# Optimization experiments

Hardware: AMD Instinct MI355X
Metric: run time of the kernel (lower is better)

## Reference

```python
import jax, jax.numpy as jnp
import numpy as np
import math

B, C, HW = 4, 256, 32          # batch, seq_len (=channels), spatial side
D_MODEL = HW * HW              # 1024
OUT_C = 32 * 32                # 1024
D_STATE = 16
EXPAND = 2
D_INNER = EXPAND * D_MODEL     # 2048
DT_RANK = math.ceil(D_MODEL / 16)  # 64
D_CONV = 4


def setup_inputs() -> dict:
    key = jax.random.key(0)
    ks = jax.random.split(key, 12)
    s = 0.02
    x1 = jax.random.normal(ks[0], (B, C, HW, HW), dtype=jnp.float32)
    in_proj_w = jax.random.normal(ks[1], (2 * D_INNER, D_MODEL), dtype=jnp.float32) * s
    conv_w = jax.random.normal(ks[2], (D_INNER, 1, D_CONV), dtype=jnp.float32) * s
    conv_b = jnp.zeros((D_INNER,), dtype=jnp.float32)
    x_proj_w = jax.random.normal(ks[3], (DT_RANK + 2 * D_STATE, D_INNER), dtype=jnp.float32) * s
    dt_proj_w = jax.random.normal(ks[4], (D_INNER, DT_RANK), dtype=jnp.float32) * s
    dt_proj_b = jnp.zeros((D_INNER,), dtype=jnp.float32)
    A_log = jnp.log(jnp.broadcast_to(jnp.arange(1, D_STATE + 1, dtype=jnp.float32), (D_INNER, D_STATE)))
    D = jnp.ones((D_INNER,), dtype=jnp.float32)
    out_proj_w = jax.random.normal(ks[5], (OUT_C, D_INNER), dtype=jnp.float32) * s
    ln_w = jnp.ones((OUT_C,), dtype=jnp.float32)
    ln_b = jnp.zeros((OUT_C,), dtype=jnp.float32)
    return {"x1": x1, "in_proj_w": in_proj_w, "conv_w": conv_w, "conv_b": conv_b,
            "x_proj_w": x_proj_w, "dt_proj_w": dt_proj_w, "dt_proj_b": dt_proj_b,
            "A_log": A_log, "D": D, "out_proj_w": out_proj_w, "ln_w": ln_w, "ln_b": ln_b}


def _mamba_forward(x, in_proj_w, conv_w, conv_b, x_proj_w, dt_proj_w, dt_proj_b, A_log, D, out_proj_w):
    # x: (B, L, d_model)
    xz = jnp.einsum('bld,ed->ble', x, in_proj_w)            # (B,L,2*d_inner)
    xs, res = jnp.split(xz, 2, axis=-1)                     # each (B,L,d_inner)
    # depthwise causal conv1d, padding=d_conv-1 then truncate to L (== left pad)
    xs_c = jnp.transpose(xs, (0, 2, 1))                     # (B,d_inner,L)
    xs_c = jax.lax.conv_general_dilated(
        xs_c, conv_w, window_strides=(1,), padding=[(D_CONV - 1, 0)],
        dimension_numbers=('NCH', 'OIH', 'NCH'), feature_group_count=D_INNER)
    xs_c = xs_c + conv_b[None, :, None]
    xs = jax.nn.silu(jnp.transpose(xs_c, (0, 2, 1)))        # (B,L,d_inner)
    # input-dependent SSM parameters
    x_dbl = jnp.einsum('bld,ed->ble', xs, x_proj_w)         # (B,L,dt_rank+2N)
    dt, Bm, Cm = jnp.split(x_dbl, [DT_RANK, DT_RANK + D_STATE], axis=-1)
    delta = jax.nn.softplus(jnp.einsum('blr,dr->bld', dt, dt_proj_w) + dt_proj_b)  # (B,L,d_inner)
    A = -jnp.exp(A_log)                                     # (d_inner, N)
    deltaA = jnp.exp(delta[..., None] * A)                  # (B,L,d_inner,N)
    deltaB_u = delta[..., None] * Bm[:, :, None, :] * xs[..., None]  # (B,L,d_inner,N)

    def step(h, inp):
        dA, dBu, Ct = inp                                   # (B,d,N),(B,d,N),(B,N)
        h = dA * h + dBu
        y = jnp.einsum('bdn,bn->bd', h, Ct)
        return h, y

    h0 = jnp.zeros((deltaA.shape[0], D_INNER, D_STATE), dtype=deltaA.dtype)
    _, ys = jax.lax.scan(step, h0, (jnp.transpose(deltaA, (1, 0, 2, 3)),
                                    jnp.transpose(deltaB_u, (1, 0, 2, 3)),
                                    jnp.transpose(Cm, (1, 0, 2))))
    y = jnp.transpose(ys, (1, 0, 2))                        # (B,L,d_inner)
    y = y + D * xs
    y = y * jax.nn.silu(res)
    return jnp.einsum('bld,od->blo', y, out_proj_w)         # (B,L,out_c)


def reference(x1, in_proj_w, conv_w, conv_b, x_proj_w, dt_proj_w, dt_proj_b,
              A_log, D, out_proj_w, ln_w, ln_b):
    b, c, h, w = x1.shape
    x = x1.reshape(b, c, h * w)                             # (B, L=c, d_model)
    y = _mamba_forward(x, in_proj_w, conv_w, conv_b, x_proj_w, dt_proj_w,
                       dt_proj_b, A_log, D, out_proj_w)
    mu = jnp.mean(y, axis=-1, keepdims=True)
    var = jnp.var(y, axis=-1, keepdims=True)
    y = (y - mu) * jax.lax.rsqrt(var + 1e-5) * ln_w + ln_b
    return y.reshape(b, c, 32, 32)
```

## Files before the change

### kernel.cpp

```cpp
#include <hip/hip_runtime.h>
#include <hip/hip_bf16.h>
#include <math.h>

#define BATCH 4
#define SEQL 256
#define DMODEL 1024
#define DINNER 2048
#define DSTATE 16
#define DTRANK 64
#define OUTC 1024
#define NROWS (BATCH * SEQL)
#define NCHUNK 4
#define CH 64

typedef __attribute__((ext_vector_type(8))) short bf16x8;
typedef __attribute__((ext_vector_type(4))) float f32x4;

__global__ __launch_bounds__(256) void gemm_mfma(const __hip_bfloat16* __restrict__ A,
                                                 const __hip_bfloat16* __restrict__ B,
                                                 float* __restrict__ C,
                                                 int M, int N, int K,
                                                 int lda, int ldb) {
    __shared__ __hip_bfloat16 As[4][128 * 32];
    __shared__ __hip_bfloat16 Bs[4][128 * 32];
    const int t  = threadIdx.x;
    const int w  = t >> 6;
    const int ln = t & 63;
    const int wm = w >> 1, wn = w & 1;
    const int q  = ln >> 4, lr = ln & 15;
    const int m0 = blockIdx.y * 128;
    const int n0 = blockIdx.x * 128;
    const int Kpart = K / gridDim.z;
    const int kbase = blockIdx.z * Kpart;

    f32x4 acc[4][4] = {};

    const __hip_bfloat16* Ag = A + (size_t)m0 * lda + kbase;
    const __hip_bfloat16* Bg = B + (size_t)n0 * ldb + kbase;

    auto stage = [&](int k0, int buf) {
        #pragma unroll
        for (int i = 0; i < 2; ++i) {
            const int c = (i * 4 + w) * 64 + ln;
            const int r = c >> 2, col = (c & 3) * 8;
            __builtin_amdgcn_global_load_lds(
                (const __attribute__((address_space(1))) void*)(Ag + (size_t)r * lda + k0 + col),
                (__attribute__((address_space(3))) void*)(As[buf] + (i * 4 + w) * 64 * 8),
                16, 0, 0);
            __builtin_amdgcn_global_load_lds(
                (const __attribute__((address_space(1))) void*)(Bg + (size_t)r * ldb + k0 + col),
                (__attribute__((address_space(3))) void*)(Bs[buf] + (i * 4 + w) * 64 * 8),
                16, 0, 0);
        }
    };

    const int nk = Kpart / 32;
    for (int s = 0; s < 3 && s < nk; ++s) stage(s * 32, s);

    for (int kk = 0; kk < nk; ++kk) {
        const int last = (kk + 2 < nk - 1) ? (kk + 2) : (nk - 1);
        const int nf = last - kk;
        if (nf >= 2)      asm volatile("s_waitcnt vmcnt(8)" ::: "memory");
        else if (nf == 1) asm volatile("s_waitcnt vmcnt(4)" ::: "memory");
        else              asm volatile("s_waitcnt vmcnt(0)" ::: "memory");
        __builtin_amdgcn_s_barrier();
        if (kk + 3 < nk) stage((kk + 3) * 32, (kk + 3) & 3);

        const int buf = kk & 3;
        bf16x8 af[4], bfr[4];
        #pragma unroll
        for (int i = 0; i < 4; ++i)
            af[i] = *(const bf16x8*)(As[buf] + (wm * 64 + i * 16 + lr) * 32 + q * 8);
        #pragma unroll
        for (int j = 0; j < 4; ++j)
            bfr[j] = *(const bf16x8*)(Bs[buf] + (wn * 64 + j * 16 + lr) * 32 + q * 8);
        #pragma unroll
        for (int i = 0; i < 4; ++i)
            #pragma unroll
            for (int j = 0; j < 4; ++j)
                acc[i][j] = __builtin_amdgcn_mfma_f32_16x16x32_bf16(af[i], bfr[j], acc[i][j], 0, 0, 0);
    }
    float* Cz = C + (size_t)blockIdx.z * M * N;
    #pragma unroll
    for (int i = 0; i < 4; ++i) {
        const int mrow = m0 + wm * 64 + i * 16 + q * 4;
        #pragma unroll
        for (int j = 0; j < 4; ++j) {
            const int ncol = n0 + wn * 64 + j * 16 + lr;
            #pragma unroll
            for (int r = 0; r < 4; ++r)
                Cz[(size_t)(mrow + r) * N + ncol] = acc[i][j][r];
        }
    }
}

__global__ __launch_bounds__(256) void gemm_dtsp(const __hip_bfloat16* __restrict__ A,
                                                 const __hip_bfloat16* __restrict__ B,
                                                 const float* __restrict__ bd,
                                                 float* __restrict__ delta) {
    __shared__ __hip_bfloat16 As[2][128 * 32];
    __shared__ __hip_bfloat16 Bs[2][128 * 32];
    const int t  = threadIdx.x;
    const int w  = t >> 6;
    const int ln = t & 63;
    const int wm = w >> 1, wn = w & 1;
    const int q  = ln >> 4, lr = ln & 15;
    const int m0 = blockIdx.y * 128;
    const int n0 = blockIdx.x * 128;
    const int lda = 128, ldb = 64, N = 2048;

    f32x4 acc[4][4] = {};
    const __hip_bfloat16* Ag = A + (size_t)m0 * lda;
    const __hip_bfloat16* Bg = B + (size_t)n0 * ldb;

    auto stage = [&](int k0, int buf) {
        #pragma unroll
        for (int i = 0; i < 2; ++i) {
            const int c = (i * 4 + w) * 64 + ln;
            const int r = c >> 2, col = (c & 3) * 8;
            __builtin_amdgcn_global_load_lds(
                (const __attribute__((address_space(1))) void*)(Ag + (size_t)r * lda + k0 + col),
                (__attribute__((address_space(3))) void*)(As[buf] + (i * 4 + w) * 64 * 8),
                16, 0, 0);
            __builtin_amdgcn_global_load_lds(
                (const __attribute__((address_space(1))) void*)(Bg + (size_t)r * ldb + k0 + col),
                (__attribute__((address_space(3))) void*)(Bs[buf] + (i * 4 + w) * 64 * 8),
                16, 0, 0);
        }
    };

    stage(0, 0);
    stage(32, 1);
    #pragma unroll
    for (int kk = 0; kk < 2; ++kk) {
        if (kk == 0) asm volatile("s_waitcnt vmcnt(4)" ::: "memory");
        else         asm volatile("s_waitcnt vmcnt(0)" ::: "memory");
        __builtin_amdgcn_s_barrier();
        bf16x8 af[4], bfr[4];
        #pragma unroll
        for (int i = 0; i < 4; ++i)
            af[i] = *(const bf16x8*)(As[kk] + (wm * 64 + i * 16 + lr) * 32 + q * 8);
        #pragma unroll
        for (int j = 0; j < 4; ++j)
            bfr[j] = *(const bf16x8*)(Bs[kk] + (wn * 64 + j * 16 + lr) * 32 + q * 8);
        #pragma unroll
        for (int i = 0; i < 4; ++i)
            #pragma unroll
            for (int j = 0; j < 4; ++j)
                acc[i][j] = __builtin_amdgcn_mfma_f32_16x16x32_bf16(af[i], bfr[j], acc[i][j], 0, 0, 0);
    }
    #pragma unroll
    for (int i = 0; i < 4; ++i) {
        const int mrow = m0 + wm * 64 + i * 16 + q * 4;
        #pragma unroll
        for (int j = 0; j < 4; ++j) {
            const int ncol = n0 + wn * 64 + j * 16 + lr;
            const float bias = bd[ncol];
            #pragma unroll
            for (int r = 0; r < 4; ++r) {
                float v = acc[i][j][r] + bias;
                float sp = (v > 20.f) ? v : log1pf(__expf(v));
                delta[(size_t)(mrow + r) * N + ncol] = sp;
            }
        }
    }
}

__global__ void xdbl_reduce_kernel(const float* __restrict__ part,
                                   float* __restrict__ xdbl,
                                   __hip_bfloat16* __restrict__ xdblb) {
    const int i = blockIdx.x * 256 + threadIdx.x;
    float s = 0.f;
    #pragma unroll
    for (int z = 0; z < 8; ++z) s += part[(size_t)z * (1024 * 128) + i];
    xdbl[i] = s;
    xdblb[i] = __float2bfloat16(s);
}

#define R0 (1024 * 1024)
#define R1 (R0 + 4096 * 1024)
#define R2 (R1 + 2048 * 1024)
#define R3 (R2 + 128 * 2048)
#define R4 (R3 + 2048 * 64)
__global__ void cast_all_kernel(const float* __restrict__ x1,
                                const float* __restrict__ w_in,
                                const float* __restrict__ w_out,
                                const float* __restrict__ w_xp,
                                const float* __restrict__ w_dt,
                                __hip_bfloat16* __restrict__ xa,
                                __hip_bfloat16* __restrict__ wb1,
                                __hip_bfloat16* __restrict__ wob,
                                __hip_bfloat16* __restrict__ wpb,
                                __hip_bfloat16* __restrict__ wdb) {
    int i = blockIdx.x * 256 + threadIdx.x;
    if (i < R0) {
        xa[i] = __float2bfloat16(x1[i]);
    } else if (i < R1) {
        int j = i - R0; wb1[j] = __float2bfloat16(w_in[j]);
    } else if (i < R2) {
        int j = i - R1; wob[j] = __float2bfloat16(w_out[j]);
    } else if (i < R3) {
        int j = i - R2; int e = j >> 11;
        wpb[j] = __float2bfloat16(e < 96 ? w_xp[j] : 0.f);
    } else if (i < R4) {
        int j = i - R3; wdb[j] = __float2bfloat16(w_dt[j]);
    }
}

__global__ void conv_silu_kernel(const float* __restrict__ xz,
                                 const float* __restrict__ conv_w,
                                 const float* __restrict__ conv_b,
                                 float* __restrict__ xs,
                                 __hip_bfloat16* __restrict__ xsb) {
    int idx = blockIdx.x * blockDim.x + threadIdx.x;
    int d = idx & (DINNER - 1);
    int l = (idx >> 11) & (SEQL - 1);
    int b = idx >> 19;
    const float w0 = conv_w[d * 4 + 0];
    const float w1 = conv_w[d * 4 + 1];
    const float w2 = conv_w[d * 4 + 2];
    const float w3 = conv_w[d * 4 + 3];
    float acc = conv_b[d];
    const size_t base = (size_t)(b * SEQL) * (2 * DINNER) + d;
    if (l >= 3) acc += w0 * xz[base + (size_t)(l - 3) * (2 * DINNER)];
    if (l >= 2) acc += w1 * xz[base + (size_t)(l - 2) * (2 * DINNER)];
    if (l >= 1) acc += w2 * xz[base + (size_t)(l - 1) * (2 * DINNER)];
    acc += w3 * xz[base + (size_t)l * (2 * DINNER)];
    float v = acc / (1.f + __expf(-acc));
    xs[idx] = v;
    xsb[idx] = __float2bfloat16(v);
}

__device__ __forceinline__ float row_reduce16(float x) {
    x += __int_as_float(__builtin_amdgcn_update_dpp(0, __float_as_int(x), 0x128, 0xF, 0xF, true));
    x += __int_as_float(__builtin_amdgcn_update_dpp(0, __float_as_int(x), 0x124, 0xF, 0xF, true));
    x += __int_as_float(__builtin_amdgcn_update_dpp(0, __float_as_int(x), 0x122, 0xF, 0xF, true));
    x += __int_as_float(__builtin_amdgcn_update_dpp(0, __float_as_int(x), 0x121, 0xF, 0xF, true));
    return x;
}

__global__ __launch_bounds__(256) void scan_carry_kernel(const float* __restrict__ delta,
                                                         const float* __restrict__ xs,
                                                         const float* __restrict__ xdbl,
                                                         const float* __restrict__ A_log,
                                                         float* __restrict__ carryL,
                                                         float* __restrict__ carryP) {
    __shared__ float sDU[CH][16][2];
    __shared__ float sB[CH][16];
    const int b = blockIdx.y, c = blockIdx.z, dg = blockIdx.x;
    const int t = threadIdx.x;
    const int dl = t >> 4, n = t & 15;
    const int d = dg * 16 + dl;
    const float a = -__expf(A_log[d * DSTATE + n]);
    const int srow = t >> 4, scol = t & 15;
    const int sd = dg * 16 + scol;
    const int rowbase = b * SEQL + c * CH;
    #pragma unroll
    for (int i = 0; i < 4; ++i) {
        const int row = rowbase + i * 16 + srow;
        const float dv = delta[(size_t)row * DINNER + sd];
        const float xv = xs[(size_t)row * DINNER + sd];
        sDU[i * 16 + srow][scol][0] = dv;
        sDU[i * 16 + srow][scol][1] = dv * xv;
        sB[i * 16 + srow][scol] = xdbl[row * 128 + 64 + scol];
    }
    __syncthreads();
    float h = 0.f, P = 1.f;
    #pragma unroll 16
    for (int l = 0; l < CH; ++l) {
        const float e = __expf(sDU[l][dl][0] * a);
        h = e * h + sDU[l][dl][1] * sB[l][n];
        P *= e;
    }
    const size_t ci = (((size_t)(b * NCHUNK + c)) * DINNER + d) * DSTATE + n;
    carryL[ci] = h;
    carryP[ci] = P;
}

__global__ __launch_bounds__(256) void scan_apply_kernel(const float* __restrict__ delta,
                                                         const float* __restrict__ xs,
                                                         const float* __restrict__ xdbl,
                                                         const float* __restrict__ xz,
                                                         const float* __restrict__ A_log,
                                                         const float* __restrict__ Dp,
                                                         const float* __restrict__ carryL,
                                                         const float* __restrict__ carryP,
                                                         __hip_bfloat16* __restrict__ ybb) {
    __shared__ float sDU[CH][16][2];
    __shared__ float sBC[CH][16][2];
    __shared__ float sGW[CH][16][2];
    const int b = blockIdx.y, c = blockIdx.z, dg = blockIdx.x;
    const int t = threadIdx.x;
    const int dl = t >> 4, n = t & 15;
    const int d = dg * 16 + dl;
    const float a = -__expf(A_log[d * DSTATE + n]);
    const int srow = t >> 4, scol = t & 15;
    const int sd = dg * 16 + scol;
    const float Dstage = Dp[sd];
    const int rowbase = b * SEQL + c * CH;
    #pragma unroll
    for (int i = 0; i < 4; ++i) {
        const int row = rowbase + i * 16 + srow;
        const float dv = delta[(size_t)row * DINNER + sd];
        const float xv = xs[(size_t)row * DINNER + sd];
        const float r  = xz[(size_t)row * (2 * DINNER) + DINNER + sd];
        const float g = r / (1.f + __expf(-r));
        const int lr_ = i * 16 + srow;
        sDU[lr_][scol][0] = dv;
        sDU[lr_][scol][1] = dv * xv;
        sGW[lr_][scol][0] = g;
        sGW[lr_][scol][1] = Dstage * xv * g;
        sBC[lr_][scol][0] = xdbl[row * 128 + 64 + scol];
        sBC[lr_][scol][1] = xdbl[row * 128 + 80 + scol];
    }
    __syncthreads();
    float h = 0.f;
    for (int j = 0; j < c; ++j) {
        const size_t ci = (((size_t)(b * NCHUNK + j)) * DINNER + d) * DSTATE + n;
        h = carryP[ci] * h + carryL[ci];
    }
    #pragma unroll 16
    for (int l = 0; l < CH; ++l) {
        const float e = __expf(sDU[l][dl][0] * a);
        h = e * h + sDU[l][dl][1] * sBC[l][n][0];
        float p = row_reduce16(h * sBC[l][n][1]);
        if (n == 0) {
            const float y = p * sGW[l][dl][0] + sGW[l][dl][1];
            ybb[(size_t)(rowbase + l) * DINNER + d] = __float2bfloat16(y);
        }
    }
}

__global__ __launch_bounds__(256) void ln_kernel(const float* __restrict__ opart,
                                                 const float* __restrict__ lw,
                                                 const float* __restrict__ lb,
                                                 float* __restrict__ out) {
    __shared__ float red[8];
    const int row = blockIdx.x;
    const int t = threadIdx.x;
    float v[4];
    float s = 0.f, s2 = 0.f;
    #pragma unroll
    for (int i = 0; i < 4; ++i) {
        const int c = t + 256 * i;
        float acc = 0.f;
        #pragma unroll
        for (int z = 0; z < 4; ++z)
            acc += opart[(size_t)z * (1024 * 1024) + (size_t)row * OUTC + c];
        v[i] = acc;
        s += acc;
        s2 += acc * acc;
    }
    #pragma unroll
    for (int o = 32; o; o >>= 1) {
        s += __shfl_down(s, o);
        s2 += __shfl_down(s2, o);
    }
    const int wid = t >> 6;
    if ((t & 63) == 0) { red[wid] = s; red[4 + wid] = s2; }
    __syncthreads();
    if (t == 0) {
        float ts = red[0] + red[1] + red[2] + red[3];
        float ts2 = red[4] + red[5] + red[6] + red[7];
        float mu = ts * (1.f / OUTC);
        float var = ts2 * (1.f / OUTC) - mu * mu;
        red[0] = mu;
        red[1] = rsqrtf(var + 1e-5f);
    }
    __syncthreads();
    const float mu = red[0], rs = red[1];
    #pragma unroll
    for (int i = 0; i < 4; ++i) {
        const int c = t + 256 * i;
        out[(size_t)row * OUTC + c] = (v[i] - mu) * rs * lw[c] + lb[c];
    }
}

extern "C" void kernel_launch(void* const* d_in, const int* in_sizes, int n_in,
                              void* d_out, int out_size, void* d_ws, size_t ws_size,
                              hipStream_t stream) {
    const float* x1        = (const float*)d_in[0];
    const float* in_proj_w = (const float*)d_in[1];
    const float* conv_w    = (const float*)d_in[2];
    const float* conv_b    = (const float*)d_in[3];
    const float* x_proj_w  = (const float*)d_in[4];
    const float* dt_proj_w = (const float*)d_in[5];
    const float* dt_proj_b = (const float*)d_in[6];
    const float* A_log     = (const float*)d_in[7];
    const float* Dp        = (const float*)d_in[8];
    const float* out_proj_w= (const float*)d_in[9];
    const float* ln_w      = (const float*)d_in[10];
    const float* ln_b      = (const float*)d_in[11];
    float* out = (float*)d_out;

    char* p = (char*)d_ws;
    __hip_bfloat16* xa    = (__hip_bfloat16*)p; p += (size_t)1024 * 1024 * 2;
    __hip_bfloat16* wb1   = (__hip_bfloat16*)p; p += (size_t)4096 * 1024 * 2;
    __hip_bfloat16* wpb   = (__hip_bfloat16*)p; p += (size_t)128 * 2048 * 2;
    __hip_bfloat16* wob   = (__hip_bfloat16*)p; p += (size_t)1024 * 2048 * 2;
    __hip_bfloat16* wdb   = (__hip_bfloat16*)p; p += (size_t)2048 * 64 * 2;
    __hip_bfloat16* xsb   = (__hip_bfloat16*)p; p += (size_t)1024 * 2048 * 2;
    __hip_bfloat16* ybb   = (__hip_bfloat16*)p; p += (size_t)1024 * 2048 * 2;
    __hip_bfloat16* xdblb = (__hip_bfloat16*)p; p += (size_t)1024 * 128 * 2;
    float* xz    = (float*)p; p += (size_t)1024 * 4096 * 4;
    float* xs    = (float*)p; p += (size_t)1024 * 2048 * 4;
    float* xdbl  = (float*)p; p += (size_t)1024 * 128 * 4;
    float* xpart = (float*)p; p += (size_t)8 * 1024 * 128 * 4;
    float* delta = (float*)p; p += (size_t)1024 * 2048 * 4;
    float* carryL = (float*)p; p += (size_t)BATCH * NCHUNK * DINNER * DSTATE * 4;
    float* carryP = (float*)p; p += (size_t)BATCH * NCHUNK * DINNER * DSTATE * 4;
    float* opart = xz;

    cast_all_kernel<<<(R4 + 255) / 256, 256, 0, stream>>>(x1, in_proj_w, out_proj_w,
                                                          x_proj_w, dt_proj_w,
                                                          xa, wb1, wob, wpb, wdb);
    gemm_mfma<<<dim3(32, 8, 1), 256, 0, stream>>>(xa, wb1, xz,
                                                  NROWS, 2 * DINNER, DMODEL, DMODEL, DMODEL);
    conv_silu_kernel<<<(NROWS * DINNER) / 256, 256, 0, stream>>>(xz, conv_w, conv_b, xs, xsb);
    gemm_mfma<<<dim3(1, 8, 8), 256, 0, stream>>>(xsb, wpb, xpart,
                                                 NROWS, 128, DINNER, DINNER, DINNER);
    xdbl_reduce_kernel<<<(1024 * 128) / 256, 256, 0, stream>>>(xpart, xdbl, xdblb);
    gemm_dtsp<<<dim3(16, 8), 256, 0, stream>>>(xdblb, wdb, dt_proj_b, delta);
    scan_carry_kernel<<<dim3(DINNER / 16, BATCH, NCHUNK), 256, 0, stream>>>(
        delta, xs, xdbl, A_log, carryL, carryP);
    scan_apply_kernel<<<dim3(DINNER / 16, BATCH, NCHUNK), 256, 0, stream>>>(
        delta, xs, xdbl, xz, A_log, Dp, carryL, carryP, ybb);
    gemm_mfma<<<dim3(8, 8, 4), 256, 0, stream>>>(ybb, wob, opart,
                                                 NROWS, OUTC, DINNER, DINNER, DINNER);
    ln_kernel<<<NROWS, 256, 0, stream>>>(opart, ln_w, ln_b, out);
}
```

Baseline: 220.0 us.

## Fuse conv+SiLU into x_proj GEMM and scan; merge chunked scan into one kernel

Removes the standalone conv_silu kernel. The depthwise causal conv and SiLU are now recomputed inside a new x_proj GEMM kernel, with split-K raised to 16, and again inside the scan. The two-pass chunked scan (carry kernel plus apply kernel) becomes one kernel that walks all four chunks sequentially per block. This drops several launches and the xs/xsb/carry buffers, at the cost of redundant conv work and fewer scan blocks (512 instead of 2048), so each block's sequential scan runs four times longer.

```diff
diff --git a/kernel.cpp b/kernel.cpp
--- a/kernel.cpp
+++ b/kernel.cpp
@@ -7,11 +7,11 @@
 #define DMODEL 1024
 #define DINNER 2048
 #define DSTATE 16
-#define DTRANK 64
 #define OUTC 1024
 #define NROWS (BATCH * SEQL)
 #define NCHUNK 4
 #define CH 64
+#define XPZ 16
 
 typedef __attribute__((ext_vector_type(8))) short bf16x8;
 typedef __attribute__((ext_vector_type(4))) float f32x4;
@@ -94,6 +94,106 @@
     }
 }
 
+__global__ __launch_bounds__(256) void xproj_conv(const float* __restrict__ xz,
+                                                  const float* __restrict__ conv_w,
+                                                  const float* __restrict__ conv_b,
+                                                  const __hip_bfloat16* __restrict__ Wp,
+                                                  float* __restrict__ xpart) {
+    __shared__ __hip_bfloat16 As[4 * 4096];
+    __shared__ __hip_bfloat16 Bs[4 * 4096];
+    const int t  = threadIdx.x;
+    const int w  = t >> 6;
+    const int ln = t & 63;
+    const int wm = w >> 1, wn = w & 1;
+    const int q  = ln >> 4, lr = ln & 15;
+    const int z  = blockIdx.x;
+    const int m0 = blockIdx.y * 128;
+    const int kbase = z * 128;
+
+    const __hip_bfloat16* Bg = Wp + kbase;
+    #pragma unroll
+    for (int stg = 0; stg < 4; ++stg) {
+        #pragma unroll
+        for (int i = 0; i < 2; ++i) {
+            const int c = (i * 4 + w) * 64 + ln;
+            const int r = c >> 2, col = (c & 3) * 8;
+            __builtin_amdgcn_global_load_lds(
+                (const __attribute__((address_space(1))) void*)(Bg + (size_t)r * 2048 + stg * 32 + col),
+                (__attribute__((address_space(3))) void*)(Bs + stg * 4096 + (i * 4 + w) * 512),
+                16, 0, 0);
+        }
+    }
+
+    {
+        const int r  = t >> 1;
+        const int dh = (t & 1) * 16;
+        const int gr = m0 + r;
+        const int bb = gr >> 8, l = gr & 255;
+        const float* xrow = xz + (size_t)bb * 256 * 4096;
+        #pragma unroll
+        for (int stg = 0; stg < 4; ++stg) {
+            const int d0 = kbase + stg * 32 + dh;
+            #pragma unroll
+            for (int j = 0; j < 4; ++j) {
+                const int d = d0 + j * 4;
+                float4 t0 = {}, t1 = {}, t2 = {}, t3;
+                if (l >= 3) t0 = *(const float4*)(xrow + (size_t)(l - 3) * 4096 + d);
+                if (l >= 2) t1 = *(const float4*)(xrow + (size_t)(l - 2) * 4096 + d);
+                if (l >= 1) t2 = *(const float4*)(xrow + (size_t)(l - 1) * 4096 + d);
+                t3 = *(const float4*)(xrow + (size_t)l * 4096 + d);
+                const float* p0 = (const float*)&t0;
+                const float* p1 = (const float*)&t1;
+                const float* p2 = (const float*)&t2;
+                const float* p3 = (const float*)&t3;
+                #pragma unroll
+                for (int u = 0; u < 4; ++u) {
+                    const int du = d + u;
+                    const float4 wv = *(const float4*)(conv_w + (size_t)du * 4);
+                    float acc = conv_b[du];
+                    if (l >= 3) acc += wv.x * p0[u];
+                    if (l >= 2) acc += wv.y * p1[u];
+                    if (l >= 1) acc += wv.z * p2[u];
+                    acc += wv.w * p3[u];
+                    const float v = acc / (1.f + __expf(-acc));
+                    As[stg * 4096 + r * 32 + dh + j * 4 + u] = __float2bfloat16(v);
+                }
+            }
+        }
+    }
+    __syncthreads();
+
+    f32x4 acc[4][4] = {};
+    #pragma unroll
+    for (int kk = 0; kk < 4; ++kk) {
+        const __hip_bfloat16* Ab = As + kk * 4096;
+        const __hip_bfloat16* Bb = Bs + kk * 4096;
+        bf16x8 af[4], bfr[4];
+        #pragma unroll
+        for (int i = 0; i < 4; ++i)
+            af[i] = *(const bf16x8*)(Ab + (wm * 64 + i * 16 + lr) * 32 + q * 8);
+        #pragma unroll
+        for (int j = 0; j < 4; ++j)
+            bfr[j] = *(const bf16x8*)(Bb + (wn * 64 + j * 16 + lr) * 32 + q * 8);
+        #pragma unroll
+        for (int i = 0; i < 4; ++i)
+            #pragma unroll
+            for (int j = 0; j < 4; ++j)
+                acc[i][j] = __builtin_amdgcn_mfma_f32_16x16x32_bf16(af[i], bfr[j], acc[i][j], 0, 0, 0);
+    }
+    float* Cz = xpart + (size_t)z * (1024 * 128);
+    #pragma unroll
+    for (int i = 0; i < 4; ++i) {
+        const int mrow = m0 + wm * 64 + i * 16 + q * 4;
+        #pragma unroll
+        for (int j = 0; j < 4; ++j) {
+            const int ncol = wn * 64 + j * 16 + lr;
+            #pragma unroll
+            for (int r = 0; r < 4; ++r)
+                Cz[(size_t)(mrow + r) * 128 + ncol] = acc[i][j][r];
+        }
+    }
+}
+
 __global__ __launch_bounds__(256) void gemm_dtsp(const __hip_bfloat16* __restrict__ A,
                                                  const __hip_bfloat16* __restrict__ B,
                                                  const float* __restrict__ bd,
@@ -172,7 +272,7 @@
     const int i = blockIdx.x * 256 + threadIdx.x;
     float s = 0.f;
     #pragma unroll
-    for (int z = 0; z < 8; ++z) s += part[(size_t)z * (1024 * 128) + i];
+    for (int z = 0; z < XPZ; ++z) s += part[(size_t)z * (1024 * 128) + i];
     xdbl[i] = s;
     xdblb[i] = __float2bfloat16(s);
 }
@@ -207,30 +307,6 @@
     }
 }
 
-__global__ void conv_silu_kernel(const float* __restrict__ xz,
-                                 const float* __restrict__ conv_w,
-                                 const float* __restrict__ conv_b,
-                                 float* __restrict__ xs,
-                                 __hip_bfloat16* __restrict__ xsb) {
-    int idx = blockIdx.x * blockDim.x + threadIdx.x;
-    int d = idx & (DINNER - 1);
-    int l = (idx >> 11) & (SEQL - 1);
-    int b = idx >> 19;
-    const float w0 = conv_w[d * 4 + 0];
-    const float w1 = conv_w[d * 4 + 1];
-    const float w2 = conv_w[d * 4 + 2];
-    const float w3 = conv_w[d * 4 + 3];
-    float acc = conv_b[d];
-    const size_t base = (size_t)(b * SEQL) * (2 * DINNER) + d;
-    if (l >= 3) acc += w0 * xz[base + (size_t)(l - 3) * (2 * DINNER)];
-    if (l >= 2) acc += w1 * xz[base + (size_t)(l - 2) * (2 * DINNER)];
-    if (l >= 1) acc += w2 * xz[base + (size_t)(l - 1) * (2 * DINNER)];
-    acc += w3 * xz[base + (size_t)l * (2 * DINNER)];
-    float v = acc / (1.f + __expf(-acc));
-    xs[idx] = v;
-    xsb[idx] = __float2bfloat16(v);
-}
-
 __device__ __forceinline__ float row_reduce16(float x) {
     x += __int_as_float(__builtin_amdgcn_update_dpp(0, __float_as_int(x), 0x128, 0xF, 0xF, true));
     x += __int_as_float(__builtin_amdgcn_update_dpp(0, __float_as_int(x), 0x124, 0xF, 0xF, true));
@@ -239,57 +315,18 @@
     return x;
 }
 
-__global__ __launch_bounds__(256) void scan_carry_kernel(const float* __restrict__ delta,
-                                                         const float* __restrict__ xs,
-                                                         const float* __restrict__ xdbl,
-                                                         const float* __restrict__ A_log,
-                                                         float* __restrict__ carryL,
-                                                         float* __restrict__ carryP) {
-    __shared__ float sDU[CH][16][2];
-    __shared__ float sB[CH][16];
-    const int b = blockIdx.y, c = blockIdx.z, dg = blockIdx.x;
-    const int t = threadIdx.x;
-    const int dl = t >> 4, n = t & 15;
-    const int d = dg * 16 + dl;
-    const float a = -__expf(A_log[d * DSTATE + n]);
-    const int srow = t >> 4, scol = t & 15;
-    const int sd = dg * 16 + scol;
-    const int rowbase = b * SEQL + c * CH;
-    #pragma unroll
-    for (int i = 0; i < 4; ++i) {
-        const int row = rowbase + i * 16 + srow;
-        const float dv = delta[(size_t)row * DINNER + sd];
-        const float xv = xs[(size_t)row * DINNER + sd];
-        sDU[i * 16 + srow][scol][0] = dv;
-        sDU[i * 16 + srow][scol][1] = dv * xv;
-        sB[i * 16 + srow][scol] = xdbl[row * 128 + 64 + scol];
-    }
-    __syncthreads();
-    float h = 0.f, P = 1.f;
-    #pragma unroll 16
-    for (int l = 0; l < CH; ++l) {
-        const float e = __expf(sDU[l][dl][0] * a);
-        h = e * h + sDU[l][dl][1] * sB[l][n];
-        P *= e;
-    }
-    const size_t ci = (((size_t)(b * NCHUNK + c)) * DINNER + d) * DSTATE + n;
-    carryL[ci] = h;
-    carryP[ci] = P;
-}
-
-__global__ __launch_bounds__(256) void scan_apply_kernel(const float* __restrict__ delta,
-                                                         const float* __restrict__ xs,
-                                                         const float* __restrict__ xdbl,
-                                                         const float* __restrict__ xz,
-                                                         const float* __restrict__ A_log,
-                                                         const float* __restrict__ Dp,
-                                                         const float* __restrict__ carryL,
-                                                         const float* __restrict__ carryP,
-                                                         __hip_bfloat16* __restrict__ ybb) {
+__global__ __launch_bounds__(256) void scan_fused(const float* __restrict__ delta,
+                                                  const float* __restrict__ xz,
+                                                  const float* __restrict__ conv_w,
+                                                  const float* __restrict__ conv_b,
+                                                  const float* __restrict__ xdbl,
+                                                  const float* __restrict__ A_log,
+                                                  const float* __restrict__ Dp,
+                                                  __hip_bfloat16* __restrict__ ybb) {
     __shared__ float sDU[CH][16][2];
     __shared__ float sBC[CH][16][2];
     __shared__ float sGW[CH][16][2];
-    const int b = blockIdx.y, c = blockIdx.z, dg = blockIdx.x;
+    const int b = blockIdx.y, dg = blockIdx.x;
     const int t = threadIdx.x;
     const int dl = t >> 4, n = t & 15;
     const int d = dg * 16 + dl;
@@ -297,36 +334,48 @@
     const int srow = t >> 4, scol = t & 15;
     const int sd = dg * 16 + scol;
     const float Dstage = Dp[sd];
-    const int rowbase = b * SEQL + c * CH;
-    #pragma unroll
-    for (int i = 0; i < 4; ++i) {
-        const int row = rowbase + i * 16 + srow;
-        const float dv = delta[(size_t)row * DINNER + sd];
-        const float xv = xs[(size_t)row * DINNER + sd];
-        const float r  = xz[(size_t)row * (2 * DINNER) + DINNER + sd];
-        const float g = r / (1.f + __expf(-r));
-        const int lr_ = i * 16 + srow;
-        sDU[lr_][scol][0] = dv;
-        sDU[lr_][scol][1] = dv * xv;
-        sGW[lr_][scol][0] = g;
-        sGW[lr_][scol][1] = Dstage * xv * g;
-        sBC[lr_][scol][0] = xdbl[row * 128 + 64 + scol];
-        sBC[lr_][scol][1] = xdbl[row * 128 + 80 + scol];
-    }
-    __syncthreads();
+    const float cb = conv_b[sd];
+    const float w0 = conv_w[sd * 4 + 0];
+    const float w1 = conv_w[sd * 4 + 1];
+    const float w2 = conv_w[sd * 4 + 2];
+    const float w3 = conv_w[sd * 4 + 3];
+    const float* xbase = xz + (size_t)(b * SEQL) * 4096 + sd;
+
     float h = 0.f;
-    for (int j = 0; j < c; ++j) {
-        const size_t ci = (((size_t)(b * NCHUNK + j)) * DINNER + d) * DSTATE + n;
-        h = carryP[ci] * h + carryL[ci];
-    }
-    #pragma unroll 16
-    for (int l = 0; l < CH; ++l) {
-        const float e = __expf(sDU[l][dl][0] * a);
-        h = e * h + sDU[l][dl][1] * sBC[l][n][0];
-        float p = row_reduce16(h * sBC[l][n][1]);
-        if (n == 0) {
-            const float y = p * sGW[l][dl][0] + sGW[l][dl][1];
-            ybb[(size_t)(rowbase + l) * DINNER + d] = __float2bfloat16(y);
+    for (int c = 0; c < NCHUNK; ++c) {
+        const int rowbase = b * SEQL + c * CH;
+        __syncthreads();
+        #pragma unroll
+        for (int i = 0; i < 4; ++i) {
+            const int row = rowbase + i * 16 + srow;
+            const int l = row & (SEQL - 1);
+            const float dv = delta[(size_t)row * DINNER + sd];
+            float acc = cb;
+            if (l >= 3) acc += w0 * xbase[(size_t)(l - 3) * 4096];
+            if (l >= 2) acc += w1 * xbase[(size_t)(l - 2) * 4096];
+            if (l >= 1) acc += w2 * xbase[(size_t)(l - 1) * 4096];
+            acc += w3 * xbase[(size_t)l * 4096];
+            const float xv = acc / (1.f + __expf(-acc));
+            const float r  = xz[(size_t)row * 4096 + DINNER + sd];
+            const float g = r / (1.f + __expf(-r));
+            const int lr_ = i * 16 + srow;
+            sDU[lr_][scol][0] = dv;
+            sDU[lr_][scol][1] = dv * xv;
+            sGW[lr_][scol][0] = g;
+            sGW[lr_][scol][1] = Dstage * xv * g;
+            sBC[lr_][scol][0] = xdbl[row * 128 + 64 + scol];
+            sBC[lr_][scol][1] = xdbl[row * 128 + 80 + scol];
+        }
+        __syncthreads();
+        #pragma unroll 16
+        for (int l = 0; l < CH; ++l) {
+            const float e = __expf(sDU[l][dl][0] * a);
+            h = e * h + sDU[l][dl][1] * sBC[l][n][0];
+            float pr = row_reduce16(h * sBC[l][n][1]);
+            if (n == 0) {
+                const float y = pr * sGW[l][dl][0] + sGW[l][dl][1];
+                ybb[(size_t)(rowbase + l) * DINNER + d] = __float2bfloat16(y);
+            }
         }
     }
 }
@@ -399,16 +448,12 @@
     __hip_bfloat16* wpb   = (__hip_bfloat16*)p; p += (size_t)128 * 2048 * 2;
     __hip_bfloat16* wob   = (__hip_bfloat16*)p; p += (size_t)1024 * 2048 * 2;
     __hip_bfloat16* wdb   = (__hip_bfloat16*)p; p += (size_t)2048 * 64 * 2;
-    __hip_bfloat16* xsb   = (__hip_bfloat16*)p; p += (size_t)1024 * 2048 * 2;
     __hip_bfloat16* ybb   = (__hip_bfloat16*)p; p += (size_t)1024 * 2048 * 2;
     __hip_bfloat16* xdblb = (__hip_bfloat16*)p; p += (size_t)1024 * 128 * 2;
     float* xz    = (float*)p; p += (size_t)1024 * 4096 * 4;
-    float* xs    = (float*)p; p += (size_t)1024 * 2048 * 4;
     float* xdbl  = (float*)p; p += (size_t)1024 * 128 * 4;
-    float* xpart = (float*)p; p += (size_t)8 * 1024 * 128 * 4;
+    float* xpart = (float*)p; p += (size_t)XPZ * 1024 * 128 * 4;
     float* delta = (float*)p; p += (size_t)1024 * 2048 * 4;
-    float* carryL = (float*)p; p += (size_t)BATCH * NCHUNK * DINNER * DSTATE * 4;
-    float* carryP = (float*)p; p += (size_t)BATCH * NCHUNK * DINNER * DSTATE * 4;
     float* opart = xz;
 
     cast_all_kernel<<<(R4 + 255) / 256, 256, 0, stream>>>(x1, in_proj_w, out_proj_w,
@@ -416,15 +461,11 @@
                                                           xa, wb1, wob, wpb, wdb);
     gemm_mfma<<<dim3(32, 8, 1), 256, 0, stream>>>(xa, wb1, xz,
                                                   NROWS, 2 * DINNER, DMODEL, DMODEL, DMODEL);
-    conv_silu_kernel<<<(NROWS * DINNER) / 256, 256, 0, stream>>>(xz, conv_w, conv_b, xs, xsb);
-    gemm_mfma<<<dim3(1, 8, 8), 256, 0, stream>>>(xsb, wpb, xpart,
-                                                 NROWS, 128, DINNER, DINNER, DINNER);
+    xproj_conv<<<dim3(XPZ, 8), 256, 0, stream>>>(xz, conv_w, conv_b, wpb, xpart);
     xdbl_reduce_kernel<<<(1024 * 128) / 256, 256, 0, stream>>>(xpart, xdbl, xdblb);
     gemm_dtsp<<<dim3(16, 8), 256, 0, stream>>>(xdblb, wdb, dt_proj_b, delta);
-    scan_carry_kernel<<<dim3(DINNER / 16, BATCH, NCHUNK), 256, 0, stream>>>(
-        delta, xs, xdbl, A_log, carryL, carryP);
-    scan_apply_kernel<<<dim3(DINNER / 16, BATCH, NCHUNK), 256, 0, stream>>>(
-        delta, xs, xdbl, xz, A_log, Dp, carryL, carryP, ybb);
+    scan_fused<<<dim3(DINNER / 16, BATCH), 256, 0, stream>>>(
+        delta, xz, conv_w, conv_b, xdbl, A_log, Dp, ybb);
     gemm_mfma<<<dim3(8, 8, 4), 256, 0, stream>>>(ybb, wob, opart,
                                                  NROWS, OUTC, DINNER, DINNER, DINNER);
     ln_kernel<<<NROWS, 256, 0, stream>>>(opart, ln_w, ln_b, out);
```

After: 237.3 us. 7.8% more time.

## Narrow GEMM tiles to 128x64, deepen split-K, vectorize casts, skip last carry chunk

Applied to the files above, without the earlier changes.

Replaces the 128x128 MFMA GEMM with a 128x64-tile variant and doubles the grid width for the in-projection and out-projection GEMMs. This puts more workgroups on the device's many compute units. The x_proj GEMM now uses split-K 16 with two N-tiles, and its reduction sums 16 partials. The cast kernel processes four floats per thread with vector loads and stores. The scan carry kernel skips the final chunk, whose carry is never consumed. Smaller tiles lower per-block arithmetic intensity and raise operand reloads, and the extra split-K adds partial-sum traffic.

```diff
diff --git a/kernel.cpp b/kernel.cpp
--- a/kernel.cpp
+++ b/kernel.cpp
@@ -7,33 +7,33 @@
 #define DMODEL 1024
 #define DINNER 2048
 #define DSTATE 16
-#define DTRANK 64
 #define OUTC 1024
 #define NROWS (BATCH * SEQL)
 #define NCHUNK 4
 #define CH 64
+#define XPZ 16
 
 typedef __attribute__((ext_vector_type(8))) short bf16x8;
 typedef __attribute__((ext_vector_type(4))) float f32x4;
 
-__global__ __launch_bounds__(256) void gemm_mfma(const __hip_bfloat16* __restrict__ A,
-                                                 const __hip_bfloat16* __restrict__ B,
-                                                 float* __restrict__ C,
-                                                 int M, int N, int K,
-                                                 int lda, int ldb) {
+__global__ __launch_bounds__(256) void gemm_n64(const __hip_bfloat16* __restrict__ A,
+                                                const __hip_bfloat16* __restrict__ B,
+                                                float* __restrict__ C,
+                                                int M, int N, int K,
+                                                int lda, int ldb) {
     __shared__ __hip_bfloat16 As[4][128 * 32];
-    __shared__ __hip_bfloat16 Bs[4][128 * 32];
+    __shared__ __hip_bfloat16 Bs[4][64 * 32];
     const int t  = threadIdx.x;
     const int w  = t >> 6;
     const int ln = t & 63;
     const int wm = w >> 1, wn = w & 1;
     const int q  = ln >> 4, lr = ln & 15;
     const int m0 = blockIdx.y * 128;
-    const int n0 = blockIdx.x * 128;
+    const int n0 = blockIdx.x * 64;
     const int Kpart = K / gridDim.z;
     const int kbase = blockIdx.z * Kpart;
 
-    f32x4 acc[4][4] = {};
+    f32x4 acc[4][2] = {};
 
     const __hip_bfloat16* Ag = A + (size_t)m0 * lda + kbase;
     const __hip_bfloat16* Bg = B + (size_t)n0 * ldb + kbase;
@@ -45,11 +45,15 @@
             const int r = c >> 2, col = (c & 3) * 8;
             __builtin_amdgcn_global_load_lds(
                 (const __attribute__((address_space(1))) void*)(Ag + (size_t)r * lda + k0 + col),
-                (__attribute__((address_space(3))) void*)(As[buf] + (i * 4 + w) * 64 * 8),
+                (__attribute__((address_space(3))) void*)(As[buf] + (i * 4 + w) * 512),
                 16, 0, 0);
+        }
+        {
+            const int c = w * 64 + ln;
+            const int r = c >> 2, col = (c & 3) * 8;
             __builtin_amdgcn_global_load_lds(
                 (const __attribute__((address_space(1))) void*)(Bg + (size_t)r * ldb + k0 + col),
-                (__attribute__((address_space(3))) void*)(Bs[buf] + (i * 4 + w) * 64 * 8),
+                (__attribute__((address_space(3))) void*)(Bs[buf] + w * 512),
                 16, 0, 0);
         }
     };
@@ -60,24 +64,24 @@
     for (int kk = 0; kk < nk; ++kk) {
         const int last = (kk + 2 < nk - 1) ? (kk + 2) : (nk - 1);
         const int nf = last - kk;
-        if (nf >= 2)      asm volatile("s_waitcnt vmcnt(8)" ::: "memory");
-        else if (nf == 1) asm volatile("s_waitcnt vmcnt(4)" ::: "memory");
+        if (nf >= 2)      asm volatile("s_waitcnt vmcnt(6)" ::: "memory");
+        else if (nf == 1) asm volatile("s_waitcnt vmcnt(3)" ::: "memory");
         else              asm volatile("s_waitcnt vmcnt(0)" ::: "memory");
         __builtin_amdgcn_s_barrier();
         if (kk + 3 < nk) stage((kk + 3) * 32, (kk + 3) & 3);
 
         const int buf = kk & 3;
-        bf16x8 af[4], bfr[4];
+        bf16x8 af[4], bfr[2];
         #pragma unroll
         for (int i = 0; i < 4; ++i)
             af[i] = *(const bf16x8*)(As[buf] + (wm * 64 + i * 16 + lr) * 32 + q * 8);
         #pragma unroll
-        for (int j = 0; j < 4; ++j)
-            bfr[j] = *(const bf16x8*)(Bs[buf] + (wn * 64 + j * 16 + lr) * 32 + q * 8);
+        for (int j = 0; j < 2; ++j)
+            bfr[j] = *(const bf16x8*)(Bs[buf] + (wn * 32 + j * 16 + lr) * 32 + q * 8);
         #pragma unroll
         for (int i = 0; i < 4; ++i)
             #pragma unroll
-            for (int j = 0; j < 4; ++j)
+            for (int j = 0; j < 2; ++j)
                 acc[i][j] = __builtin_amdgcn_mfma_f32_16x16x32_bf16(af[i], bfr[j], acc[i][j], 0, 0, 0);
     }
     float* Cz = C + (size_t)blockIdx.z * M * N;
@@ -85,8 +89,8 @@
     for (int i = 0; i < 4; ++i) {
         const int mrow = m0 + wm * 64 + i * 16 + q * 4;
         #pragma unroll
-        for (int j = 0; j < 4; ++j) {
-            const int ncol = n0 + wn * 64 + j * 16 + lr;
+        for (int j = 0; j < 2; ++j) {
+            const int ncol = n0 + wn * 32 + j * 16 + lr;
             #pragma unroll
             for (int r = 0; r < 4; ++r)
                 Cz[(size_t)(mrow + r) * N + ncol] = acc[i][j][r];
@@ -172,7 +176,7 @@
     const int i = blockIdx.x * 256 + threadIdx.x;
     float s = 0.f;
     #pragma unroll
-    for (int z = 0; z < 8; ++z) s += part[(size_t)z * (1024 * 128) + i];
+    for (int z = 0; z < XPZ; ++z) s += part[(size_t)z * (1024 * 128) + i];
     xdbl[i] = s;
     xdblb[i] = __float2bfloat16(s);
 }
@@ -182,6 +186,20 @@
 #define R2 (R1 + 2048 * 1024)
 #define R3 (R2 + 128 * 2048)
 #define R4 (R3 + 2048 * 64)
+
+__device__ __forceinline__ ushort4 cvt4(float4 v) {
+    __hip_bfloat16 h0 = __float2bfloat16(v.x);
+    __hip_bfloat16 h1 = __float2bfloat16(v.y);
+    __hip_bfloat16 h2 = __float2bfloat16(v.z);
+    __hip_bfloat16 h3 = __float2bfloat16(v.w);
+    ushort4 o;
+    o.x = *reinterpret_cast<unsigned short*>(&h0);
+    o.y = *reinterpret_cast<unsigned short*>(&h1);
+    o.z = *reinterpret_cast<unsigned short*>(&h2);
+    o.w = *reinterpret_cast<unsigned short*>(&h3);
+    return o;
+}
+
 __global__ void cast_all_kernel(const float* __restrict__ x1,
                                 const float* __restrict__ w_in,
                                 const float* __restrict__ w_out,
@@ -192,18 +210,23 @@
                                 __hip_bfloat16* __restrict__ wob,
                                 __hip_bfloat16* __restrict__ wpb,
                                 __hip_bfloat16* __restrict__ wdb) {
-    int i = blockIdx.x * 256 + threadIdx.x;
+    const int i = (blockIdx.x * 256 + threadIdx.x) * 4;
+    if (i >= R4) return;
     if (i < R0) {
-        xa[i] = __float2bfloat16(x1[i]);
+        *reinterpret_cast<ushort4*>(xa + i) = cvt4(*(const float4*)(x1 + i));
     } else if (i < R1) {
-        int j = i - R0; wb1[j] = __float2bfloat16(w_in[j]);
+        int j = i - R0;
+        *reinterpret_cast<ushort4*>(wb1 + j) = cvt4(*(const float4*)(w_in + j));
     } else if (i < R2) {
-        int j = i - R1; wob[j] = __float2bfloat16(w_out[j]);
+        int j = i - R1;
+        *reinterpret_cast<ushort4*>(wob + j) = cvt4(*(const float4*)(w_out + j));
     } else if (i < R3) {
         int j = i - R2; int e = j >> 11;
-        wpb[j] = __float2bfloat16(e < 96 ? w_xp[j] : 0.f);
-    } else if (i < R4) {
-        int j = i - R3; wdb[j] = __float2bfloat16(w_dt[j]);
+        float4 v = (e < 96) ? *(const float4*)(w_xp + j) : float4{0.f, 0.f, 0.f, 0.f};
+        *reinterpret_cast<ushort4*>(wpb + j) = cvt4(v);
+    } else {
+        int j = i - R3;
+        *reinterpret_cast<ushort4*>(wdb + j) = cvt4(*(const float4*)(w_dt + j));
     }
 }
 
@@ -323,9 +346,9 @@
     for (int l = 0; l < CH; ++l) {
         const float e = __expf(sDU[l][dl][0] * a);
         h = e * h + sDU[l][dl][1] * sBC[l][n][0];
-        float p = row_reduce16(h * sBC[l][n][1]);
+        float pr = row_reduce16(h * sBC[l][n][1]);
         if (n == 0) {
-            const float y = p * sGW[l][dl][0] + sGW[l][dl][1];
+            const float y = pr * sGW[l][dl][0] + sGW[l][dl][1];
             ybb[(size_t)(rowbase + l) * DINNER + d] = __float2bfloat16(y);
         }
     }
@@ -405,27 +428,27 @@
     float* xz    = (float*)p; p += (size_t)1024 * 4096 * 4;
     float* xs    = (float*)p; p += (size_t)1024 * 2048 * 4;
     float* xdbl  = (float*)p; p += (size_t)1024 * 128 * 4;
-    float* xpart = (float*)p; p += (size_t)8 * 1024 * 128 * 4;
+    float* xpart = (float*)p; p += (size_t)XPZ * 1024 * 128 * 4;
     float* delta = (float*)p; p += (size_t)1024 * 2048 * 4;
     float* carryL = (float*)p; p += (size_t)BATCH * NCHUNK * DINNER * DSTATE * 4;
     float* carryP = (float*)p; p += (size_t)BATCH * NCHUNK * DINNER * DSTATE * 4;
     float* opart = xz;
 
-    cast_all_kernel<<<(R4 + 255) / 256, 256, 0, stream>>>(x1, in_proj_w, out_proj_w,
-                                                          x_proj_w, dt_proj_w,
-                                                          xa, wb1, wob, wpb, wdb);
-    gemm_mfma<<<dim3(32, 8, 1), 256, 0, stream>>>(xa, wb1, xz,
-                                                  NROWS, 2 * DINNER, DMODEL, DMODEL, DMODEL);
+    cast_all_kernel<<<(R4 / 4 + 255) / 256, 256, 0, stream>>>(x1, in_proj_w, out_proj_w,
+                                                              x_proj_w, dt_proj_w,
+                                                              xa, wb1, wob, wpb, wdb);
+    gemm_n64<<<dim3(64, 8, 1), 256, 0, stream>>>(xa, wb1, xz,
+                                                 NROWS, 2 * DINNER, DMODEL, DMODEL, DMODEL);
     conv_silu_kernel<<<(NROWS * DINNER) / 256, 256, 0, stream>>>(xz, conv_w, conv_b, xs, xsb);
-    gemm_mfma<<<dim3(1, 8, 8), 256, 0, stream>>>(xsb, wpb, xpart,
-                                                 NROWS, 128, DINNER, DINNER, DINNER);
+    gemm_n64<<<dim3(2, 8, XPZ), 256, 0, stream>>>(xsb, wpb, xpart,
+                                                  NROWS, 128, DINNER, DINNER, DINNER);
     xdbl_reduce_kernel<<<(1024 * 128) / 256, 256, 0, stream>>>(xpart, xdbl, xdblb);
     gemm_dtsp<<<dim3(16, 8), 256, 0, stream>>>(xdblb, wdb, dt_proj_b, delta);
-    scan_carry_kernel<<<dim3(DINNER / 16, BATCH, NCHUNK), 256, 0, stream>>>(
+    scan_carry_kernel<<<dim3(DINNER / 16, BATCH, NCHUNK - 1), 256, 0, stream>>>(
         delta, xs, xdbl, A_log, carryL, carryP);
     scan_apply_kernel<<<dim3(DINNER / 16, BATCH, NCHUNK), 256, 0, stream>>>(
         delta, xs, xdbl, xz, A_log, Dp, carryL, carryP, ybb);
-    gemm_mfma<<<dim3(8, 8, 4), 256, 0, stream>>>(ybb, wob, opart,
+    gemm_n64<<<dim3(16, 8, 4), 256, 0, stream>>>(ybb, wob, opart,
                                                  NROWS, OUTC, DINNER, DINNER, DINNER);
     ln_kernel<<<NROWS, 256, 0, stream>>>(opart, ln_w, ln_b, out);
 }
```

New measurement: 209.3 us. 1.05x faster.
